# Performance work log

Measured on AMD Instinct MI355X. Metric: run time of the kernel, lower is better.

The kernel has to match this reference:

```python
import jax, jax.numpy as jnp
import numpy as np

C = 32
C_Z = 128
S = 256
N_SEQ = 256
LN_EPS = 1e-5


def setup_inputs() -> dict:
    key = jax.random.key(0)
    k1, k2, k3, k4 = jax.random.split(key, 4)
    m_si = jax.random.normal(k1, (S, N_SEQ, C), dtype=jnp.float32)
    ln_gamma = jnp.ones((C,), dtype=jnp.float32)
    ln_beta = jnp.zeros((C,), dtype=jnp.float32)
    # nn.Linear(c, 2c, bias=False): weight shape (2c, c)
    W_ab = jax.random.normal(k2, (2 * C, C), dtype=jnp.float32) / np.sqrt(C)
    # nn.Linear(c*c, c_z): weight (c_z, c*c), bias (c_z,)
    W_out = jax.random.normal(k3, (C_Z, C * C), dtype=jnp.float32) / np.sqrt(C * C)
    b_out = jax.random.normal(k4, (C_Z,), dtype=jnp.float32) * 0.01
    return {"m_si": m_si, "ln_gamma": ln_gamma, "ln_beta": ln_beta,
            "W_ab": W_ab, "W_out": W_out, "b_out": b_out}


def reference(m_si, ln_gamma, ln_beta, W_ab, W_out, b_out):
    # LayerNorm over channel dim c
    mu = jnp.mean(m_si, axis=-1, keepdims=True)
    var = jnp.var(m_si, axis=-1, keepdims=True)
    x = (m_si - mu) * jax.lax.rsqrt(var + LN_EPS) * ln_gamma + ln_beta
    # linear_no_bias then chunk into a, b: each (s, n_seq, c)
    ab = jnp.einsum('snc,dc->snd', x, W_ab)
    a, b = ab[..., :C], ab[..., C:]
    # mean over MSA sequences of outer products a[s,i,:] x b[s,j,:]
    # restructured as a contraction over n_seq: (i, j, c, c)
    outer = jnp.einsum('inc,jnd->ijcd', a, b) / N_SEQ
    outer = outer.reshape(S, S, C * C)  # flatten (c, c) -> c*c
    # final linear projection to c_z
    z_ij = jnp.einsum('ijk,zk->ijz', outer, W_out) + b_out
    return z_ij
```

## Files before the change

### kernel.cpp

```cpp
#include <hip/hip_runtime.h>

#define SDIM 256
#define NSEQ 256
#define CDIM 32
#define CZ 128
#define IB 8
#define JB 4

typedef __bf16 bfx8 __attribute__((ext_vector_type(8)));
typedef float fx4 __attribute__((ext_vector_type(4)));
typedef float f32x16 __attribute__((ext_vector_type(16)));
typedef unsigned int u32x4 __attribute__((ext_vector_type(4)));

__device__ __forceinline__ unsigned short f2bf(float f) {
  unsigned int u = __float_as_uint(f);
  u += 0x7fffu + ((u >> 16) & 1u);
  return (unsigned short)(u >> 16);
}

__device__ __forceinline__ unsigned int cvtpk(float lo, float hi) {
  unsigned int r;
  asm("v_cvt_pk_bf16_f32 %0, %1, %2" : "=v"(r) : "v"(lo), "v"(hi));
  return r;
}

__device__ __forceinline__ bfx8 pack8(const fx4 lo, const fx4 hi) {
  bfx8 r;
  r[0] = (__bf16)lo[0]; r[1] = (__bf16)lo[1]; r[2] = (__bf16)lo[2]; r[3] = (__bf16)lo[3];
  r[4] = (__bf16)hi[0]; r[5] = (__bf16)hi[1]; r[6] = (__bf16)hi[2]; r[7] = (__bf16)hi[3];
  return r;
}

__device__ __forceinline__ void gload16(const void* g, void* l) {
  __builtin_amdgcn_global_load_lds((const __attribute__((address_space(1))) unsigned int*)g,
                                   (__attribute__((address_space(3))) unsigned int*)l,
                                   16, 0, 0);
}


__global__ __launch_bounds__(256) void opm_prep(
    const float* __restrict__ m_si, const float* __restrict__ gamma, const float* __restrict__ beta,
    const float* __restrict__ Wab, const float* __restrict__ Wout,
    unsigned short* __restrict__ a_t, unsigned short* __restrict__ b_t,
    unsigned short* __restrict__ w2T)
{
  __shared__ __align__(16) char shbuf[8192];
  const int b = blockIdx.x;
  const int t = threadIdx.x;
  if (b < SDIM) {
    const int s = b;
    const int l = t & 63;
    const int w = t >> 6;
    const int nl = l & 15;
    const int cg = l >> 4;

    bfx8 afr[4];
#pragma unroll
    for (int dt = 0; dt < 4; ++dt) {
      const float* wr = Wab + (dt * 16 + nl) * 32 + cg * 8;
      afr[dt] = pack8(*(const fx4*)wr, *(const fx4*)(wr + 4));
    }
    const fx4 g0 = *(const fx4*)(gamma + cg * 8);
    const fx4 g1 = *(const fx4*)(gamma + cg * 8 + 4);
    const fx4 bt0 = *(const fx4*)(beta + cg * 8);
    const fx4 bt1 = *(const fx4*)(beta + cg * 8 + 4);

#pragma unroll
    for (int p = 0; p < 4; ++p) {
      const int n = p * 64 + w * 16 + nl;
      const float* xr = m_si + (s * 256 + n) * 32 + cg * 8;
      const fx4 v0 = *(const fx4*)xr;
      const fx4 v1 = *(const fx4*)(xr + 4);
      float ps  = v0[0] + v0[1] + v0[2] + v0[3] + v1[0] + v1[1] + v1[2] + v1[3];
      float ps2 = v0[0]*v0[0] + v0[1]*v0[1] + v0[2]*v0[2] + v0[3]*v0[3]
                + v1[0]*v1[0] + v1[1]*v1[1] + v1[2]*v1[2] + v1[3]*v1[3];
      ps  += __shfl_xor(ps, 16);  ps  += __shfl_xor(ps, 32);
      ps2 += __shfl_xor(ps2, 16); ps2 += __shfl_xor(ps2, 32);
      const float mu = ps * 0.03125f;
      const float var = ps2 * 0.03125f - mu * mu;
      const float inv = rsqrtf(var + 1e-5f);
      const fx4 e0 = (v0 - mu) * inv * g0 + bt0;
      const fx4 e1 = (v1 - mu) * inv * g1 + bt1;
      const bfx8 bfr = pack8(e0, e1);

      fx4 dz[4];
#pragma unroll
      for (int dt = 0; dt < 4; ++dt)
        dz[dt] = __builtin_amdgcn_mfma_f32_16x16x32_bf16(afr[dt], bfr, (fx4){0.f,0.f,0.f,0.f}, 0, 0, 0);

#pragma unroll
      for (int dt = 0; dt < 4; ++dt) {
#pragma unroll
        for (int r = 0; r < 4; ++r) {
          const int d = dt * 16 + cg * 4 + r;
          const unsigned short hv = f2bf(dz[dt][r]);
          if (d < 32) a_t[(s * 32 + d) * 256 + n] = hv;
          else        b_t[(s * 32 + (d - 32)) * 256 + n] = hv;
        }
      }
    }
  } else {
    unsigned short* lin = (unsigned short*)shbuf;
    const int blk = b - SDIM;
    const float* wsrc = Wout + blk * 4096;
#pragma unroll
    for (int jj = 0; jj < 4; ++jj) {
      const int q = t + jj * 256;
      const fx4 v = ((const fx4*)wsrc)[q];
      unsigned short* dst = lin + q * 4;
      dst[0] = f2bf(v[0]); dst[1] = f2bf(v[1]); dst[2] = f2bf(v[2]); dst[3] = f2bf(v[3]);
    }
    __syncthreads();
    const int z0 = blk * 4;
#pragma unroll
    for (int w = 0; w < 2; ++w) {
      const int id = t + w * 256;
      const int lz = id & 3;
      const int hh = (id >> 2) & 1;
      const int ks = id >> 3;
      const int z = z0 + lz;
      unsigned short vals[8];
#pragma unroll
      for (int e = 0; e < 8; ++e) {
        const int kp = ks * 16 + hh * 8 + e;
        const int c = (kp & 3) | (((kp >> 8) & 1) << 2) | (((kp >> 2) & 1) << 3) | (((kp >> 9) & 1) << 4);
        const int d = (kp >> 3) & 31;
        vals[e] = lin[lz * 1024 + c * CDIM + d];
      }
      const int dest = ((z >> 5) << 15) + (ks << 9) + (hh << 8) + ((z & 31) << 3);
      *(u32x4*)(w2T + dest) = *(const u32x4*)vals;
    }
  }
}

__global__ __launch_bounds__(512, 4) void opm_main(
    const unsigned short* __restrict__ a_t, const unsigned short* __restrict__ b_t,
    const unsigned short* __restrict__ w2T, const float* __restrict__ bout,
    float* __restrict__ out)
{
  __shared__ __align__(16) char smem[73728];
  char* o_sh = smem;

  const int tid = threadIdx.x;
  const int lane = tid & 63;
  const int wid = tid >> 6;
  const int l31 = lane & 31;
  const int h = lane >> 5;

  const int bxr = blockIdx.x;
  const int xc = bxr & 7;
  const int q8 = bxr >> 3;
  const int it = q8 >> 4;
  const int jt = q8 & 15;
  const int i0 = ((xc & 1) * 16 + it) * IB;
  const int j0 = ((xc >> 1) * 16 + jt) * JB;

  const int wm = wid >> 1;
  const int wn = wid & 1;
  const int wbase = wid * 1024;

  f32x16 acc00 = {}, acc01 = {}, acc10 = {}, acc11 = {};

  auto STAGE_A = [&](int buf, int nc) {
    const int nbase = nc * 32;
    char* A = smem + buf * 16384;
#pragma unroll
    for (int pass = 0; pass < 2; ++pass) {
      const int q = pass * 512 + tid;
      const int row = q >> 2;
      const int gs = (q & 3) ^ ((q >> 3) & 3);
      const unsigned short* src = a_t + ((i0 + (row >> 5)) * 32 + (row & 31)) * 256 + nbase + gs * 8;
      gload16(src, A + pass * 8192 + wbase);
    }
  };
  auto STAGE_B = [&](int buf, int nc) {
    const int nbase = nc * 32;
    char* B = smem + 49152 + buf * 8192;
    const int q = tid;
    const int row = q >> 2;
    const int gs = (q & 3) ^ ((q >> 3) & 3);
    const unsigned short* src = b_t + ((j0 + (row >> 5)) * 32 + (row & 31)) * 256 + nbase + gs * 8;
    gload16(src, B + wbase);
  };

  auto HALF = [&](int buf, int ks) {
    char* A = smem + buf * 16384;
    char* B = smem + 49152 + buf * 8192;
    const int s = ks * 2 + h;
    bfx8 af0, af1, bf0, bf1;
    { const int r = wm * 64 + l31;      af0 = *(const bfx8*)(A + r * 64 + (((s ^ (r >> 1)) & 3) << 4)); }
    { const int r = wm * 64 + 32 + l31; af1 = *(const bfx8*)(A + r * 64 + (((s ^ (r >> 1)) & 3) << 4)); }
    { const int r = wn * 64 + l31;      bf0 = *(const bfx8*)(B + r * 64 + (((s ^ (r >> 1)) & 3) << 4)); }
    { const int r = wn * 64 + 32 + l31; bf1 = *(const bfx8*)(B + r * 64 + (((s ^ (r >> 1)) & 3) << 4)); }
    __builtin_amdgcn_s_setprio(1);
    acc00 = __builtin_amdgcn_mfma_f32_32x32x16_bf16(af0, bf0, acc00, 0, 0, 0);
    acc01 = __builtin_amdgcn_mfma_f32_32x32x16_bf16(af0, bf1, acc01, 0, 0, 0);
    acc10 = __builtin_amdgcn_mfma_f32_32x32x16_bf16(af1, bf0, acc10, 0, 0, 0);
    acc11 = __builtin_amdgcn_mfma_f32_32x32x16_bf16(af1, bf1, acc11, 0, 0, 0);
    __builtin_amdgcn_s_setprio(0);
  };

  STAGE_A(0, 0); STAGE_B(0, 0);
  STAGE_A(1, 1); STAGE_B(1, 1);

#pragma unroll
  for (int c = 0; c < 8; ++c) {
    const int buf = c % 3;
    if (c + 2 < 8) STAGE_A((c + 2) % 3, c + 2);
    if (c <= 5)      { asm volatile("s_waitcnt vmcnt(5)" ::: "memory"); }
    else if (c == 6) { asm volatile("s_waitcnt vmcnt(3)" ::: "memory"); }
    else             { asm volatile("s_waitcnt vmcnt(0)" ::: "memory"); }
    __builtin_amdgcn_s_barrier();
    asm volatile("" ::: "memory");
    HALF(buf, 0);
    asm volatile("s_waitcnt lgkmcnt(0)" ::: "memory");
    __builtin_amdgcn_s_barrier();
    if (c + 2 < 8) STAGE_B((c + 2) % 3, c + 2);
    asm volatile("" ::: "memory");
    HALF(buf, 1);
    asm volatile("s_waitcnt lgkmcnt(0)" ::: "memory");
    __builtin_amdgcn_s_barrier();
  }
  __syncthreads();

  {
    const f32x16 av[4] = { acc00 * 0.00390625f, acc01 * 0.00390625f,
                           acc10 * 0.00390625f, acc11 * 0.00390625f };
#pragma unroll
    for (int mi = 0; mi < 2; ++mi) {
#pragma unroll
      for (int ni = 0; ni < 2; ++ni) {
        const f32x16 a = av[mi * 2 + ni];
        const int p = (wm * 2 + mi) * 4 + (wn * 2 + ni);
#pragma unroll
        for (int c4 = 0; c4 < 2; ++c4) {
          const int sl = l31 + 32 * h + 64 * c4;
          u32x4 v;
          v[0] = cvtpk(a[8 * c4 + 0], a[8 * c4 + 1]);
          v[1] = cvtpk(a[8 * c4 + 2], a[8 * c4 + 3]);
          v[2] = cvtpk(a[8 * c4 + 4], a[8 * c4 + 5]);
          v[3] = cvtpk(a[8 * c4 + 6], a[8 * c4 + 7]);
          *(u32x4*)(o_sh + p * 2048 + ((sl ^ (p & 7)) << 4)) = v;
        }
      }
    }
  }
  __syncthreads();

  {
    const int ztp = wid & 1;
    const int kh = wid >> 1;
    const unsigned short* wpa = w2T + ((ztp * 2 + 0) << 15) + (h << 8) + (l31 << 3);
    const unsigned short* wpb = w2T + ((ztp * 2 + 1) << 15) + (h << 8) + (l31 << 3);
    const int obase = l31 * 2048;
    const int oxor = l31 & 7;
    const int ks0 = kh * 16;

    bfx8 wa[4], wb[4];
#pragma unroll
    for (int q = 0; q < 4; ++q) {
      wa[q] = *(const bfx8*)(wpa + ((ks0 + q) << 9));
      wb[q] = *(const bfx8*)(wpb + ((ks0 + q) << 9));
    }
    bfx8 oc = *(const bfx8*)(o_sh + obase + ((((ks0 << 1) + h) ^ oxor) << 4));
    bfx8 on = *(const bfx8*)(o_sh + obase + (((((ks0 + 1) << 1) + h) ^ oxor) << 4));

    f32x16 za = {}, zb = {};
#pragma unroll
    for (int st = 0; st < 16; ++st) {
      const int q = st & 3;
      __builtin_amdgcn_s_setprio(1);
      za = __builtin_amdgcn_mfma_f32_32x32x16_bf16(wa[q], oc, za, 0, 0, 0);
      zb = __builtin_amdgcn_mfma_f32_32x32x16_bf16(wb[q], oc, zb, 0, 0, 0);
      __builtin_amdgcn_s_setprio(0);
      oc = on;
      if (st < 14) on = *(const bfx8*)(o_sh + obase + (((((ks0 + st + 2) << 1) + h) ^ oxor) << 4));
      if (st < 12) {
        wa[q] = *(const bfx8*)(wpa + ((ks0 + st + 4) << 9));
        wb[q] = *(const bfx8*)(wpb + ((ks0 + st + 4) << 9));
      }
    }
    __syncthreads();

    const int slot = (kh >> 1) * 2 + ztp;
    auto PWRITE = [&](char* base) {
#pragma unroll
      for (int zs = 0; zs < 2; ++zs) {
        const f32x16& A = zs ? zb : za;
#pragma unroll
        for (int g2 = 0; g2 < 4; ++g2) {
          fx4 v = { A[4 * g2], A[4 * g2 + 1], A[4 * g2 + 2], A[4 * g2 + 3] };
          *(fx4*)(base + zs * 4096 + (((g2 * 2 + h) * 32 + l31) << 4)) = v;
        }
      }
    };
    auto PADD = [&](const char* base) {
#pragma unroll
      for (int zs = 0; zs < 2; ++zs) {
        f32x16& A = zs ? zb : za;
#pragma unroll
        for (int g2 = 0; g2 < 4; ++g2) {
          const fx4 v = *(const fx4*)(base + zs * 4096 + (((g2 * 2 + h) * 32 + l31) << 4));
          A[4 * g2 + 0] += v[0]; A[4 * g2 + 1] += v[1];
          A[4 * g2 + 2] += v[2]; A[4 * g2 + 3] += v[3];
        }
      }
    };
    if (kh & 1) PWRITE(o_sh + slot * 8192);
    __syncthreads();
    if (!(kh & 1)) {
      PADD(o_sh + slot * 8192);
      if (kh == 2) PWRITE(o_sh + 32768 + ztp * 8192);
    }
    __syncthreads();
    if (kh == 0) {
      PADD(o_sh + 32768 + ztp * 8192);
      const int i = i0 + (l31 >> 2), j = j0 + (l31 & 3);
      float* op = out + (i * SDIM + j) * CZ + ztp * 64;
      const float* bp = bout + ztp * 64;
#pragma unroll
      for (int zs = 0; zs < 2; ++zs) {
        const f32x16& A = zs ? zb : za;
#pragma unroll
        for (int g2 = 0; g2 < 4; ++g2) {
          const int zl = zs * 32 + g2 * 8 + h * 4;
          fx4 v = { A[4 * g2], A[4 * g2 + 1], A[4 * g2 + 2], A[4 * g2 + 3] };
          v += *(const fx4*)(bp + zl);
          *(fx4*)(op + zl) = v;
        }
      }
    }
  }
}

extern "C" void kernel_launch(void* const* d_in, const int* in_sizes, int n_in,
                              void* d_out, int out_size, void* d_ws, size_t ws_size,
                              hipStream_t stream) {
  const float* m_si  = (const float*)d_in[0];
  const float* gamma = (const float*)d_in[1];
  const float* beta  = (const float*)d_in[2];
  const float* Wab   = (const float*)d_in[3];
  const float* Wout  = (const float*)d_in[4];
  const float* bout  = (const float*)d_in[5];
  float* out = (float*)d_out;

  char* ws = (char*)d_ws;
  unsigned short* a_t = (unsigned short*)ws;
  unsigned short* b_t = (unsigned short*)(ws + (4u << 20));
  unsigned short* w2T = (unsigned short*)(ws + (8u << 20));

  opm_prep<<<dim3(SDIM + 32), dim3(256), 0, stream>>>(m_si, gamma, beta, Wab, Wout, a_t, b_t, w2T);
  opm_main<<<dim3(2048), dim3(512), 0, stream>>>(a_t, b_t, w2T, bout, out);
}
```

Before: 74.99 us.

## Enlarge main-kernel tile to 8x8 pairs to improve operand reuse

```diff
diff --git a/kernel.cpp b/kernel.cpp
--- a/kernel.cpp
+++ b/kernel.cpp
@@ -5,7 +5,7 @@
 #define CDIM 32
 #define CZ 128
 #define IB 8
-#define JB 4
+#define JB 8
 
 typedef __bf16 bfx8 __attribute__((ext_vector_type(8)));
 typedef float fx4 __attribute__((ext_vector_type(4)));
@@ -133,12 +133,12 @@
   }
 }
 
-__global__ __launch_bounds__(512, 4) void opm_main(
+__global__ __launch_bounds__(512, 2) void opm_main(
     const unsigned short* __restrict__ a_t, const unsigned short* __restrict__ b_t,
     const unsigned short* __restrict__ w2T, const float* __restrict__ bout,
     float* __restrict__ out)
 {
-  __shared__ __align__(16) char smem[73728];
+  __shared__ __align__(16) char smem[131072];
   char* o_sh = smem;
 
   const int tid = threadIdx.x;
@@ -149,17 +149,18 @@
 
   const int bxr = blockIdx.x;
   const int xc = bxr & 7;
-  const int q8 = bxr >> 3;
-  const int it = q8 >> 4;
-  const int jt = q8 & 15;
-  const int i0 = ((xc & 1) * 16 + it) * IB;
-  const int j0 = ((xc >> 1) * 16 + jt) * JB;
-
-  const int wm = wid >> 1;
-  const int wn = wid & 1;
+  const int q7 = bxr >> 3;
+  const int it = (xc & 3) * 8 + (q7 >> 4);
+  const int jt = (xc >> 2) * 16 + (q7 & 15);
+  const int i0 = it * IB;
+  const int j0 = jt * JB;
+
+  const int wm = wid >> 2;
+  const int wn = wid & 3;
   const int wbase = wid * 1024;
 
   f32x16 acc00 = {}, acc01 = {}, acc10 = {}, acc11 = {};
+  f32x16 acc20 = {}, acc21 = {}, acc30 = {}, acc31 = {};
 
   auto STAGE_A = [&](int buf, int nc) {
     const int nbase = nc * 32;
@@ -175,28 +176,37 @@
   };
   auto STAGE_B = [&](int buf, int nc) {
     const int nbase = nc * 32;
-    char* B = smem + 49152 + buf * 8192;
-    const int q = tid;
-    const int row = q >> 2;
-    const int gs = (q & 3) ^ ((q >> 3) & 3);
-    const unsigned short* src = b_t + ((j0 + (row >> 5)) * 32 + (row & 31)) * 256 + nbase + gs * 8;
-    gload16(src, B + wbase);
+    char* B = smem + 49152 + buf * 16384;
+#pragma unroll
+    for (int pass = 0; pass < 2; ++pass) {
+      const int q = pass * 512 + tid;
+      const int row = q >> 2;
+      const int gs = (q & 3) ^ ((q >> 3) & 3);
+      const unsigned short* src = b_t + ((j0 + (row >> 5)) * 32 + (row & 31)) * 256 + nbase + gs * 8;
+      gload16(src, B + pass * 8192 + wbase);
+    }
   };
 
   auto HALF = [&](int buf, int ks) {
     char* A = smem + buf * 16384;
-    char* B = smem + 49152 + buf * 8192;
+    char* B = smem + 49152 + buf * 16384;
     const int s = ks * 2 + h;
-    bfx8 af0, af1, bf0, bf1;
-    { const int r = wm * 64 + l31;      af0 = *(const bfx8*)(A + r * 64 + (((s ^ (r >> 1)) & 3) << 4)); }
-    { const int r = wm * 64 + 32 + l31; af1 = *(const bfx8*)(A + r * 64 + (((s ^ (r >> 1)) & 3) << 4)); }
-    { const int r = wn * 64 + l31;      bf0 = *(const bfx8*)(B + r * 64 + (((s ^ (r >> 1)) & 3) << 4)); }
-    { const int r = wn * 64 + 32 + l31; bf1 = *(const bfx8*)(B + r * 64 + (((s ^ (r >> 1)) & 3) << 4)); }
+    bfx8 af0, af1, af2, af3, bf0, bf1;
+    { const int r = wm * 128 +  0 + l31; af0 = *(const bfx8*)(A + r * 64 + (((s ^ (r >> 1)) & 3) << 4)); }
+    { const int r = wm * 128 + 32 + l31; af1 = *(const bfx8*)(A + r * 64 + (((s ^ (r >> 1)) & 3) << 4)); }
+    { const int r = wm * 128 + 64 + l31; af2 = *(const bfx8*)(A + r * 64 + (((s ^ (r >> 1)) & 3) << 4)); }
+    { const int r = wm * 128 + 96 + l31; af3 = *(const bfx8*)(A + r * 64 + (((s ^ (r >> 1)) & 3) << 4)); }
+    { const int r = wn * 64 + l31;       bf0 = *(const bfx8*)(B + r * 64 + (((s ^ (r >> 1)) & 3) << 4)); }
+    { const int r = wn * 64 + 32 + l31;  bf1 = *(const bfx8*)(B + r * 64 + (((s ^ (r >> 1)) & 3) << 4)); }
     __builtin_amdgcn_s_setprio(1);
     acc00 = __builtin_amdgcn_mfma_f32_32x32x16_bf16(af0, bf0, acc00, 0, 0, 0);
     acc01 = __builtin_amdgcn_mfma_f32_32x32x16_bf16(af0, bf1, acc01, 0, 0, 0);
     acc10 = __builtin_amdgcn_mfma_f32_32x32x16_bf16(af1, bf0, acc10, 0, 0, 0);
     acc11 = __builtin_amdgcn_mfma_f32_32x32x16_bf16(af1, bf1, acc11, 0, 0, 0);
+    acc20 = __builtin_amdgcn_mfma_f32_32x32x16_bf16(af2, bf0, acc20, 0, 0, 0);
+    acc21 = __builtin_amdgcn_mfma_f32_32x32x16_bf16(af2, bf1, acc21, 0, 0, 0);
+    acc30 = __builtin_amdgcn_mfma_f32_32x32x16_bf16(af3, bf0, acc30, 0, 0, 0);
+    acc31 = __builtin_amdgcn_mfma_f32_32x32x16_bf16(af3, bf1, acc31, 0, 0, 0);
     __builtin_amdgcn_s_setprio(0);
   };
 
@@ -207,8 +217,8 @@
   for (int c = 0; c < 8; ++c) {
     const int buf = c % 3;
     if (c + 2 < 8) STAGE_A((c + 2) % 3, c + 2);
-    if (c <= 5)      { asm volatile("s_waitcnt vmcnt(5)" ::: "memory"); }
-    else if (c == 6) { asm volatile("s_waitcnt vmcnt(3)" ::: "memory"); }
+    if (c <= 5)      { asm volatile("s_waitcnt vmcnt(6)" ::: "memory"); }
+    else if (c == 6) { asm volatile("s_waitcnt vmcnt(4)" ::: "memory"); }
     else             { asm volatile("s_waitcnt vmcnt(0)" ::: "memory"); }
     __builtin_amdgcn_s_barrier();
     asm volatile("" ::: "memory");
@@ -224,14 +234,16 @@
   __syncthreads();
 
   {
-    const f32x16 av[4] = { acc00 * 0.00390625f, acc01 * 0.00390625f,
-                           acc10 * 0.00390625f, acc11 * 0.00390625f };
-#pragma unroll
-    for (int mi = 0; mi < 2; ++mi) {
+    const f32x16 av[8] = { acc00 * 0.00390625f, acc01 * 0.00390625f,
+                           acc10 * 0.00390625f, acc11 * 0.00390625f,
+                           acc20 * 0.00390625f, acc21 * 0.00390625f,
+                           acc30 * 0.00390625f, acc31 * 0.00390625f };
+#pragma unroll
+    for (int sub = 0; sub < 4; ++sub) {
 #pragma unroll
       for (int ni = 0; ni < 2; ++ni) {
-        const f32x16 a = av[mi * 2 + ni];
-        const int p = (wm * 2 + mi) * 4 + (wn * 2 + ni);
+        const f32x16 a = av[sub * 2 + ni];
+        const int p = (wm * 4 + sub) * 8 + (wn * 2 + ni);
 #pragma unroll
         for (int c4 = 0; c4 < 2; ++c4) {
           const int sl = l31 + 32 * h + 64 * c4;
@@ -252,8 +264,10 @@
     const int kh = wid >> 1;
     const unsigned short* wpa = w2T + ((ztp * 2 + 0) << 15) + (h << 8) + (l31 << 3);
     const unsigned short* wpb = w2T + ((ztp * 2 + 1) << 15) + (h << 8) + (l31 << 3);
-    const int obase = l31 * 2048;
-    const int oxor = l31 & 7;
+    const int p0 = l31;
+    const int p1 = 32 + l31;
+    const int ob0 = p0 * 2048, ox0 = p0 & 7;
+    const int ob1 = p1 * 2048, ox1 = p1 & 7;
     const int ks0 = kh * 16;
 
     bfx8 wa[4], wb[4];
@@ -262,19 +276,27 @@
       wa[q] = *(const bfx8*)(wpa + ((ks0 + q) << 9));
       wb[q] = *(const bfx8*)(wpb + ((ks0 + q) << 9));
     }
-    bfx8 oc = *(const bfx8*)(o_sh + obase + ((((ks0 << 1) + h) ^ oxor) << 4));
-    bfx8 on = *(const bfx8*)(o_sh + obase + (((((ks0 + 1) << 1) + h) ^ oxor) << 4));
-
-    f32x16 za = {}, zb = {};
+    bfx8 oc0 = *(const bfx8*)(o_sh + ob0 + ((((ks0 << 1) + h) ^ ox0) << 4));
+    bfx8 on0 = *(const bfx8*)(o_sh + ob0 + (((((ks0 + 1) << 1) + h) ^ ox0) << 4));
+    bfx8 oc1 = *(const bfx8*)(o_sh + ob1 + ((((ks0 << 1) + h) ^ ox1) << 4));
+    bfx8 on1 = *(const bfx8*)(o_sh + ob1 + (((((ks0 + 1) << 1) + h) ^ ox1) << 4));
+
+    f32x16 za0 = {}, zb0 = {}, za1 = {}, zb1 = {};
 #pragma unroll
     for (int st = 0; st < 16; ++st) {
       const int q = st & 3;
       __builtin_amdgcn_s_setprio(1);
-      za = __builtin_amdgcn_mfma_f32_32x32x16_bf16(wa[q], oc, za, 0, 0, 0);
-      zb = __builtin_amdgcn_mfma_f32_32x32x16_bf16(wb[q], oc, zb, 0, 0, 0);
+      za0 = __builtin_amdgcn_mfma_f32_32x32x16_bf16(wa[q], oc0, za0, 0, 0, 0);
+      zb0 = __builtin_amdgcn_mfma_f32_32x32x16_bf16(wb[q], oc0, zb0, 0, 0, 0);
+      za1 = __builtin_amdgcn_mfma_f32_32x32x16_bf16(wa[q], oc1, za1, 0, 0, 0);
+      zb1 = __builtin_amdgcn_mfma_f32_32x32x16_bf16(wb[q], oc1, zb1, 0, 0, 0);
       __builtin_amdgcn_s_setprio(0);
-      oc = on;
-      if (st < 14) on = *(const bfx8*)(o_sh + obase + (((((ks0 + st + 2) << 1) + h) ^ oxor) << 4));
+      oc0 = on0; oc1 = on1;
+      if (st < 14) {
+        const int sl = ((ks0 + st + 2) << 1) + h;
+        on0 = *(const bfx8*)(o_sh + ob0 + ((sl ^ ox0) << 4));
+        on1 = *(const bfx8*)(o_sh + ob1 + ((sl ^ ox1) << 4));
+      }
       if (st < 12) {
         wa[q] = *(const bfx8*)(wpa + ((ks0 + st + 4) << 9));
         wb[q] = *(const bfx8*)(wpb + ((ks0 + st + 4) << 9));
@@ -286,47 +308,58 @@
     auto PWRITE = [&](char* base) {
 #pragma unroll
       for (int zs = 0; zs < 2; ++zs) {
-        const f32x16& A = zs ? zb : za;
+        const f32x16& A0 = zs ? zb0 : za0;
+        const f32x16& A1 = zs ? zb1 : za1;
 #pragma unroll
         for (int g2 = 0; g2 < 4; ++g2) {
-          fx4 v = { A[4 * g2], A[4 * g2 + 1], A[4 * g2 + 2], A[4 * g2 + 3] };
-          *(fx4*)(base + zs * 4096 + (((g2 * 2 + h) * 32 + l31) << 4)) = v;
+          fx4 v0 = { A0[4 * g2], A0[4 * g2 + 1], A0[4 * g2 + 2], A0[4 * g2 + 3] };
+          fx4 v1 = { A1[4 * g2], A1[4 * g2 + 1], A1[4 * g2 + 2], A1[4 * g2 + 3] };
+          *(fx4*)(base + zs * 8192 + (((g2 * 2 + h) * 64 + p0) << 4)) = v0;
+          *(fx4*)(base + zs * 8192 + (((g2 * 2 + h) * 64 + p1) << 4)) = v1;
         }
       }
     };
     auto PADD = [&](const char* base) {
 #pragma unroll
       for (int zs = 0; zs < 2; ++zs) {
-        f32x16& A = zs ? zb : za;
+        f32x16& A0 = zs ? zb0 : za0;
+        f32x16& A1 = zs ? zb1 : za1;
 #pragma unroll
         for (int g2 = 0; g2 < 4; ++g2) {
-          const fx4 v = *(const fx4*)(base + zs * 4096 + (((g2 * 2 + h) * 32 + l31) << 4));
-          A[4 * g2 + 0] += v[0]; A[4 * g2 + 1] += v[1];
-          A[4 * g2 + 2] += v[2]; A[4 * g2 + 3] += v[3];
+          const fx4 v0 = *(const fx4*)(base + zs * 8192 + (((g2 * 2 + h) * 64 + p0) << 4));
+          const fx4 v1 = *(const fx4*)(base + zs * 8192 + (((g2 * 2 + h) * 64 + p1) << 4));
+          A0[4 * g2 + 0] += v0[0]; A0[4 * g2 + 1] += v0[1];
+          A0[4 * g2 + 2] += v0[2]; A0[4 * g2 + 3] += v0[3];
+          A1[4 * g2 + 0] += v1[0]; A1[4 * g2 + 1] += v1[1];
+          A1[4 * g2 + 2] += v1[2]; A1[4 * g2 + 3] += v1[3];
         }
       }
     };
-    if (kh & 1) PWRITE(o_sh + slot * 8192);
+    if (kh & 1) PWRITE(o_sh + slot * 16384);
     __syncthreads();
     if (!(kh & 1)) {
-      PADD(o_sh + slot * 8192);
-      if (kh == 2) PWRITE(o_sh + 32768 + ztp * 8192);
+      PADD(o_sh + slot * 16384);
+      if (kh == 2) PWRITE(o_sh + 65536 + ztp * 16384);
     }
     __syncthreads();
     if (kh == 0) {
-      PADD(o_sh + 32768 + ztp * 8192);
-      const int i = i0 + (l31 >> 2), j = j0 + (l31 & 3);
-      float* op = out + (i * SDIM + j) * CZ + ztp * 64;
+      PADD(o_sh + 65536 + ztp * 16384);
       const float* bp = bout + ztp * 64;
 #pragma unroll
-      for (int zs = 0; zs < 2; ++zs) {
-        const f32x16& A = zs ? zb : za;
-#pragma unroll
-        for (int g2 = 0; g2 < 4; ++g2) {
-          const int zl = zs * 32 + g2 * 8 + h * 4;
-          fx4 v = { A[4 * g2], A[4 * g2 + 1], A[4 * g2 + 2], A[4 * g2 + 3] };
-          v += *(const fx4*)(bp + zl);
-          *(fx4*)(op + zl) = v;
+      for (int pg = 0; pg < 2; ++pg) {
+        const int p = pg * 32 + l31;
+        const int i = i0 + (p >> 3), j = j0 + (p & 7);
+        float* op = out + (i * SDIM + j) * CZ + ztp * 64;
+#pragma unroll
+        for (int zs = 0; zs < 2; ++zs) {
+          const f32x16& A = zs ? (pg ? zb1 : zb0) : (pg ? za1 : za0);
+#pragma unroll
+          for (int g2 = 0; g2 < 4; ++g2) {
+            const int zl = zs * 32 + g2 * 8 + h * 4;
+            fx4 v = { A[4 * g2], A[4 * g2 + 1], A[4 * g2 + 2], A[4 * g2 + 3] };
+            v += *(const fx4*)(bp + zl);
+            *(fx4*)(op + zl) = v;
+          }
         }
       }
     }
@@ -350,5 +383,5 @@
   unsigned short* w2T = (unsigned short*)(ws + (8u << 20));
 
   opm_prep<<<dim3(SDIM + 32), dim3(256), 0, stream>>>(m_si, gamma, beta, Wab, Wout, a_t, b_t, w2T);
-  opm_main<<<dim3(2048), dim3(512), 0, stream>>>(a_t, b_t, w2T, bout, out);
-}
+  opm_main<<<dim3(1024), dim3(512), 0, stream>>>(a_t, b_t, w2T, bout, out);
+}
```

After: 73.10 us. 1.03x faster.

## Enlarge main kernel tile to 8x8 (i,j) pairs with 1024-thread blocks

Applied to the files above, without the earlier changes.

```diff
diff --git a/kernel.cpp b/kernel.cpp
--- a/kernel.cpp
+++ b/kernel.cpp
@@ -5,7 +5,7 @@
 #define CDIM 32
 #define CZ 128
 #define IB 8
-#define JB 4
+#define JB 8
 
 typedef __bf16 bfx8 __attribute__((ext_vector_type(8)));
 typedef float fx4 __attribute__((ext_vector_type(4)));
@@ -133,12 +133,12 @@
   }
 }
 
-__global__ __launch_bounds__(512, 4) void opm_main(
+__global__ __launch_bounds__(1024, 4) void opm_main(
     const unsigned short* __restrict__ a_t, const unsigned short* __restrict__ b_t,
     const unsigned short* __restrict__ w2T, const float* __restrict__ bout,
     float* __restrict__ out)
 {
-  __shared__ __align__(16) char smem[73728];
+  __shared__ __align__(16) char smem[131072];
   char* o_sh = smem;
 
   const int tid = threadIdx.x;
@@ -149,14 +149,14 @@
 
   const int bxr = blockIdx.x;
   const int xc = bxr & 7;
-  const int q8 = bxr >> 3;
-  const int it = q8 >> 4;
-  const int jt = q8 & 15;
-  const int i0 = ((xc & 1) * 16 + it) * IB;
-  const int j0 = ((xc >> 1) * 16 + jt) * JB;
-
-  const int wm = wid >> 1;
-  const int wn = wid & 1;
+  const int q7 = bxr >> 3;
+  const int it = (xc & 3) * 8 + (q7 >> 4);
+  const int jt = (xc >> 2) * 16 + (q7 & 15);
+  const int i0 = it * IB;
+  const int j0 = jt * JB;
+
+  const int wm = wid >> 2;
+  const int wn = wid & 3;
   const int wbase = wid * 1024;
 
   f32x16 acc00 = {}, acc01 = {}, acc10 = {}, acc11 = {};
@@ -164,18 +164,15 @@
   auto STAGE_A = [&](int buf, int nc) {
     const int nbase = nc * 32;
     char* A = smem + buf * 16384;
-#pragma unroll
-    for (int pass = 0; pass < 2; ++pass) {
-      const int q = pass * 512 + tid;
-      const int row = q >> 2;
-      const int gs = (q & 3) ^ ((q >> 3) & 3);
-      const unsigned short* src = a_t + ((i0 + (row >> 5)) * 32 + (row & 31)) * 256 + nbase + gs * 8;
-      gload16(src, A + pass * 8192 + wbase);
-    }
+    const int q = tid;
+    const int row = q >> 2;
+    const int gs = (q & 3) ^ ((q >> 3) & 3);
+    const unsigned short* src = a_t + ((i0 + (row >> 5)) * 32 + (row & 31)) * 256 + nbase + gs * 8;
+    gload16(src, A + wbase);
   };
   auto STAGE_B = [&](int buf, int nc) {
     const int nbase = nc * 32;
-    char* B = smem + 49152 + buf * 8192;
+    char* B = smem + 49152 + buf * 16384;
     const int q = tid;
     const int row = q >> 2;
     const int gs = (q & 3) ^ ((q >> 3) & 3);
@@ -185,7 +182,7 @@
 
   auto HALF = [&](int buf, int ks) {
     char* A = smem + buf * 16384;
-    char* B = smem + 49152 + buf * 8192;
+    char* B = smem + 49152 + buf * 16384;
     const int s = ks * 2 + h;
     bfx8 af0, af1, bf0, bf1;
     { const int r = wm * 64 + l31;      af0 = *(const bfx8*)(A + r * 64 + (((s ^ (r >> 1)) & 3) << 4)); }
@@ -207,8 +204,8 @@
   for (int c = 0; c < 8; ++c) {
     const int buf = c % 3;
     if (c + 2 < 8) STAGE_A((c + 2) % 3, c + 2);
-    if (c <= 5)      { asm volatile("s_waitcnt vmcnt(5)" ::: "memory"); }
-    else if (c == 6) { asm volatile("s_waitcnt vmcnt(3)" ::: "memory"); }
+    if (c <= 5)      { asm volatile("s_waitcnt vmcnt(3)" ::: "memory"); }
+    else if (c == 6) { asm volatile("s_waitcnt vmcnt(2)" ::: "memory"); }
     else             { asm volatile("s_waitcnt vmcnt(0)" ::: "memory"); }
     __builtin_amdgcn_s_barrier();
     asm volatile("" ::: "memory");
@@ -231,7 +228,7 @@
 #pragma unroll
       for (int ni = 0; ni < 2; ++ni) {
         const f32x16 a = av[mi * 2 + ni];
-        const int p = (wm * 2 + mi) * 4 + (wn * 2 + ni);
+        const int p = (wm * 2 + mi) * 8 + (wn * 2 + ni);
 #pragma unroll
         for (int c4 = 0; c4 < 2; ++c4) {
           const int sl = l31 + 32 * h + 64 * c4;
@@ -249,11 +246,13 @@
 
   {
     const int ztp = wid & 1;
-    const int kh = wid >> 1;
+    const int kh = (wid >> 1) & 3;
+    const int pg = wid >> 3;
     const unsigned short* wpa = w2T + ((ztp * 2 + 0) << 15) + (h << 8) + (l31 << 3);
     const unsigned short* wpb = w2T + ((ztp * 2 + 1) << 15) + (h << 8) + (l31 << 3);
-    const int obase = l31 * 2048;
-    const int oxor = l31 & 7;
+    const int p = pg * 32 + l31;
+    const int obase = p * 2048;
+    const int oxor = p & 7;
     const int ks0 = kh * 16;
 
     bfx8 wa[4], wb[4];
@@ -290,7 +289,7 @@
 #pragma unroll
         for (int g2 = 0; g2 < 4; ++g2) {
           fx4 v = { A[4 * g2], A[4 * g2 + 1], A[4 * g2 + 2], A[4 * g2 + 3] };
-          *(fx4*)(base + zs * 4096 + (((g2 * 2 + h) * 32 + l31) << 4)) = v;
+          *(fx4*)(base + zs * 8192 + (((g2 * 2 + h) * 64 + p) << 4)) = v;
         }
       }
     };
@@ -300,24 +299,24 @@
         f32x16& A = zs ? zb : za;
 #pragma unroll
         for (int g2 = 0; g2 < 4; ++g2) {
-          const fx4 v = *(const fx4*)(base + zs * 4096 + (((g2 * 2 + h) * 32 + l31) << 4));
+          const fx4 v = *(const fx4*)(base + zs * 8192 + (((g2 * 2 + h) * 64 + p) << 4));
           A[4 * g2 + 0] += v[0]; A[4 * g2 + 1] += v[1];
           A[4 * g2 + 2] += v[2]; A[4 * g2 + 3] += v[3];
         }
       }
     };
-    if (kh & 1) PWRITE(o_sh + slot * 8192);
+    if (kh & 1) PWRITE(o_sh + slot * 16384);
     __syncthreads();
     if (!(kh & 1)) {
-      PADD(o_sh + slot * 8192);
-      if (kh == 2) PWRITE(o_sh + 32768 + ztp * 8192);
+      PADD(o_sh + slot * 16384);
+      if (kh == 2) PWRITE(o_sh + 65536 + ztp * 16384);
     }
     __syncthreads();
     if (kh == 0) {
-      PADD(o_sh + 32768 + ztp * 8192);
-      const int i = i0 + (l31 >> 2), j = j0 + (l31 & 3);
+      PADD(o_sh + 65536 + ztp * 16384);
+      const float* bp = bout + ztp * 64;
+      const int i = i0 + (p >> 3), j = j0 + (p & 7);
       float* op = out + (i * SDIM + j) * CZ + ztp * 64;
-      const float* bp = bout + ztp * 64;
 #pragma unroll
       for (int zs = 0; zs < 2; ++zs) {
         const f32x16& A = zs ? zb : za;
@@ -350,5 +349,5 @@
   unsigned short* w2T = (unsigned short*)(ws + (8u << 20));
 
   opm_prep<<<dim3(SDIM + 32), dim3(256), 0, stream>>>(m_si, gamma, beta, Wab, Wout, a_t, b_t, w2T);
-  opm_main<<<dim3(2048), dim3(512), 0, stream>>>(a_t, b_t, w2T, bout, out);
-}
+  opm_main<<<dim3(1024), dim3(1024), 0, stream>>>(a_t, b_t, w2T, bout, out);
+}
```

Result: slower. 81.78 us (+9.1%).
